# Kernel tuning notes

Hardware: AMD Instinct MI355X
Metric: run time of the kernel (lower is better)

The kernel has to match this reference:

```python
import jax, jax.numpy as jnp
import numpy as np

N_NODE = 100000
HIDDEN = 128
BATCH = 4096
SESS_LEN = 50


def setup_inputs() -> dict:
    key = jax.random.key(0)
    k1, k2, k3, k4, k5 = jax.random.split(key, 5)
    return {
        "item_embedding": jax.random.normal(k1, (N_NODE, HIDDEN), dtype=jnp.float32),
        "items": jax.random.randint(k2, (BATCH, SESS_LEN), 0, N_NODE, dtype=jnp.int64),
        "A": jax.random.uniform(k3, (BATCH, BATCH), dtype=jnp.float32),
        "D": jax.random.uniform(k4, (BATCH, BATCH), dtype=jnp.float32),
        "target_embedding": jax.random.normal(k5, (BATCH, 1, 2 * HIDDEN), dtype=jnp.float32),
    }


def reference(item_embedding, items, A, D, target_embedding):
    # Gather per-session item embeddings: (batch, sess_len, hidden)
    seq_h = item_embedding[items]
    # Sum over session positions -> (batch, hidden)
    relation_emb = jnp.sum(seq_h, axis=1)
    # DA = D @ A, then propagate: (batch, batch) @ (batch, hidden)
    DA = jnp.matmul(D, A)
    relation_emb = jnp.matmul(DA, relation_emb)
    # Row-wise L2 normalization (torch.norm(dim=-1))
    norm = jnp.linalg.norm(relation_emb, axis=-1, keepdims=True)
    return relation_emb / norm
```

## Files before the change

### kernel.cpp

```cpp
#include <hip/hip_runtime.h>
#include <hip/hip_bf16.h>

#define BATCH   4096
#define HIDDEN  128
#define SESS    50
#define KTOT    4096
#define NB      ((size_t)BATCH * HIDDEN)

#define BK      128
#define NT      16
#define ABYTES  16384
#define BBYTES  32768
#define BUF     (ABYTES + BBYTES)

typedef __bf16 bf16x8 __attribute__((ext_vector_type(8)));
typedef __bf16 bf16x4 __attribute__((ext_vector_type(4)));
typedef float  f32x4  __attribute__((ext_vector_type(4)));
typedef float  f32x2  __attribute__((ext_vector_type(2)));

__device__ __forceinline__ f32x4 mfma_bf16(bf16x8 a, bf16x8 b, f32x4 c) {
    return __builtin_amdgcn_mfma_f32_16x16x32_bf16(a, b, c, 0, 0, 0);
}

__device__ __forceinline__ void gload16(const void* g, void* l) {
    __builtin_amdgcn_global_load_lds(
        (const __attribute__((address_space(1))) void*)g,
        (__attribute__((address_space(3))) void*)l, 16, 0, 0);
}


__global__ __launch_bounds__(256)
void gather_sum_kernel(const float* __restrict__ emb,
                       const int* __restrict__ items32,
                       __bf16* __restrict__ ETp) {
    __shared__ int sidx[4][SESS];
    const int t  = threadIdx.x;
    const int b0 = blockIdx.x * 4;
    const bool is64 = (items32[1] | items32[3] | items32[5] | items32[7] |
                       items32[9] | items32[11] | items32[13] | items32[15]) == 0;
    if (t < 4 * SESS) {
        const int w_ = t / SESS, s_ = t % SESS;
        sidx[w_][s_] = is64
            ? (int)((const long long*)items32)[(long)(b0 + w_) * SESS + s_]
            : items32[(b0 + w_) * SESS + s_];
    }
    __syncthreads();
    const int w    = t >> 6;
    const int lane = t & 63;
    const int c    = lane & 31;
    const int h    = lane >> 5;
    f32x4 acc = {0.f, 0.f, 0.f, 0.f};
#pragma unroll
    for (int i = 0; i < 25; ++i) {
        acc += *(const f32x4*)(emb + (long)sidx[w][h + 2 * i] * HIDDEN + c * 4);
    }
#pragma unroll
    for (int j = 0; j < 4; ++j) acc[j] += __shfl_xor(acc[j], 32, 64);
    if (h == 0) {
        const int  b     = b0 + w;
        const long chunk = b >> 3;
        const int  swz   = (int)((chunk & 3) << 4);
        char* basep = (char*)ETp + chunk * 2048 + (b & 7) * 2;
        const int hi4 = (c >> 2) * 256;
#pragma unroll
        for (int j = 0; j < 4; ++j) {
            const int hl = 4 * (c & 3) + j;
            *(__bf16*)(basep + ((hi4 + hl * 16) ^ swz)) = (__bf16)acc[j];
        }
    }
}

__global__ __launch_bounds__(256, 1)
void gemm_mfma_kernel(const float* __restrict__ X,
                      const __bf16* __restrict__ Bpk,
                      float* __restrict__ Tpart) {
    __shared__ __align__(16) char lds[3 * BUF];
    const int tid  = threadIdx.x;
    const int w    = tid >> 6;
    const int lane = tid & 63;
    const int lo   = lane & 15;
    const int quad = lane >> 4;
    const int rowBase = blockIdx.x * 32;
    const int kh      = blockIdx.y;

#define STAGE(t_, dst_) do {                                                 \
    _Pragma("unroll")                                                        \
    for (int ai_ = 0; ai_ < 4; ++ai_) {                                      \
        const int i_    = 4 * w + ai_;                                       \
        const int rloc_ = 2 * i_ + (lane >> 5);                              \
        gload16((const char*)X +                                             \
                    ((size_t)(rowBase + rloc_) * KTOT + kh * 2048 +          \
                     (size_t)(t_) * BK) * 4 +                                \
                    (((lane & 31) * 16) ^ ((rloc_ & 7) << 4)),               \
                (dst_) + i_ * 1024);                                         \
    }                                                                        \
    _Pragma("unroll")                                                        \
    for (int bi_ = 0; bi_ < 8; ++bi_) {                                      \
        const int j_ = 8 * w + bi_;                                          \
        gload16((const char*)Bpk + (size_t)kh * 524288 +                     \
                    (size_t)(t_) * BBYTES + j_ * 1024 + lane * 16,           \
                (dst_) + ABYTES + j_ * 1024);                                \
    }                                                                        \
} while (0)

    f32x4 acc[4];
#pragma unroll
    for (int i = 0; i < 4; ++i) acc[i] = (f32x4){0.f, 0.f, 0.f, 0.f};

    const int rbase = (w & 1) * 16;
    const int ntb   = (w >> 1) * 4;
    const int akey  = (lo & 7) << 4;
    const int bkey  = quad << 4;

#define KTILE(cb_) do {                                                      \
    const char* Ar_ = (cb_) + (rbase + lo) * 512;                            \
    const char* Bb_ = (cb_) + ABYTES + quad * 2048;                          \
    _Pragma("unroll")                                                        \
    for (int ks_ = 0; ks_ < 4; ++ks_) {                                      \
        const f32x4 a0_ =                                                    \
            *(const f32x4*)(Ar_ + ((ks_ * 128 + quad * 32) ^ akey));         \
        const f32x4 a1_ =                                                    \
            *(const f32x4*)(Ar_ + ((ks_ * 128 + quad * 32 + 16) ^ akey));    \
        bf16x8 af_;                                                          \
        af_[0] = (__bf16)a0_[0]; af_[1] = (__bf16)a0_[1];                    \
        af_[2] = (__bf16)a0_[2]; af_[3] = (__bf16)a0_[3];                    \
        af_[4] = (__bf16)a1_[0]; af_[5] = (__bf16)a1_[1];                    \
        af_[6] = (__bf16)a1_[2]; af_[7] = (__bf16)a1_[3];                    \
        _Pragma("unroll")                                                    \
        for (int j_ = 0; j_ < 4; ++j_) {                                     \
            const bf16x8 b_ = *(const bf16x8*)(Bb_ + ks_ * 8192 +            \
                (((ntb + j_) * 256 + lo * 16) ^ bkey));                      \
            acc[j_] = mfma_bf16(af_, b_, acc[j_]);                           \
        }                                                                    \
    }                                                                        \
} while (0)

    STAGE(0, lds);
    STAGE(1, lds + BUF);

    char* cb = lds;
    char* sb = lds + 2 * BUF;
    for (int t = 0; t < NT; ++t) {
        if (t + 2 < NT) STAGE(t + 2, sb);
        if (t < NT - 2)
            asm volatile("s_waitcnt vmcnt(24)" ::: "memory");
        else if (t == NT - 2)
            asm volatile("s_waitcnt vmcnt(12)" ::: "memory");
        else
            asm volatile("s_waitcnt vmcnt(0)" ::: "memory");
        __builtin_amdgcn_s_barrier();
        __builtin_amdgcn_sched_barrier(0);
        KTILE(cb);
        __builtin_amdgcn_s_barrier();
        __builtin_amdgcn_sched_barrier(0);
        cb += BUF; if (cb == lds + 3 * BUF) cb = lds;
        sb += BUF; if (sb == lds + 3 * BUF) sb = lds;
    }
#undef KTILE
#undef STAGE

    float* op = Tpart + (size_t)kh * NB +
                (size_t)(rowBase + rbase) * HIDDEN;
#pragma unroll
    for (int r = 0; r < 4; ++r) {
#pragma unroll
        for (int j = 0; j < 4; ++j)
            op[(quad * 4 + r) * HIDDEN + (ntb + j) * 16 + lo] = acc[j][r];
    }
}

__global__ __launch_bounds__(256)
void reduce2_kernel(const float* __restrict__ Tp, __bf16* __restrict__ TTp) {
    const size_t i = ((size_t)blockIdx.x * 256 + threadIdx.x) * 4;
    f32x4 a = *(const f32x4*)(Tp + i);
    a += *(const f32x4*)(Tp + NB + i);
    const int  b     = (int)(i >> 7);
    const int  h0    = (int)(i & 127);
    const long chunk = b >> 3;
    const int  swz   = (int)((chunk & 3) << 4);
    char* basep = (char*)TTp + chunk * 2048 + (b & 7) * 2;
#pragma unroll
    for (int j = 0; j < 4; ++j) {
        const int h = h0 + j;
        *(__bf16*)(basep + (((h >> 4) * 256 + (h & 15) * 16) ^ swz)) =
            (__bf16)a[j];
    }
}

__global__ __launch_bounds__(256)
void reduce_norm_kernel(const float* __restrict__ Tp, float* __restrict__ out) {
    const int t    = threadIdx.x;
    const int w    = t >> 6;
    const int lane = t & 63;
    const int row  = blockIdx.x * 4 + w;
    const size_t base = (size_t)row * HIDDEN + lane * 2;
    f32x2 v = *(const f32x2*)(Tp + base);
    v += *(const f32x2*)(Tp + NB + base);
    float sq = v[0] * v[0] + v[1] * v[1];
#pragma unroll
    for (int m = 1; m < 64; m <<= 1) sq += __shfl_xor(sq, m, 64);
    const float s = rsqrtf(sq);
    f32x2 o = {v[0] * s, v[1] * s};
    *(f32x2*)(out + base) = o;
}

extern "C" void kernel_launch(void* const* d_in, const int* in_sizes, int n_in,
                              void* d_out, int out_size, void* d_ws, size_t ws_size,
                              hipStream_t stream) {
    const float* emb   = (const float*)d_in[0];
    const int*   items = (const int*)d_in[1];
    const float* A     = (const float*)d_in[2];
    const float* D     = (const float*)d_in[3];
    float* out = (float*)d_out;

    __bf16* ETp = (__bf16*)d_ws;
    __bf16* TTp = ETp + NB;
    float*  Tp  = (float*)(TTp + NB);

    gather_sum_kernel<<<BATCH / 4, 256, 0, stream>>>(emb, items, ETp);
    gemm_mfma_kernel<<<dim3(BATCH / 32, 2), 256, 0, stream>>>(A, ETp, Tp);
    reduce2_kernel<<<512, 256, 0, stream>>>(Tp, TTp);
    gemm_mfma_kernel<<<dim3(BATCH / 32, 2), 256, 0, stream>>>(D, TTp, Tp);
    reduce_norm_kernel<<<BATCH / 4, 256, 0, stream>>>(Tp, out);
}
```

Before: 209.8 us.

## Retile GEMM to 64-row blocks with four-way split-K and 64-wide K tiles

Each GEMM workgroup now covers 64 rows instead of 32, and every wave computes a full 16x128 output strip. K is split four ways instead of two, and the K tile shrinks to 64, so each staged buffer holds less data. Each B tile loaded into LDS is now reused by twice as many rows, while the grid stays at 256 workgroups. In exchange the split-K partials double, so the reduce and normalize kernels read four partial buffers, which adds global memory traffic and workspace.

```diff
diff --git a/kernel.cpp b/kernel.cpp
--- a/kernel.cpp
+++ b/kernel.cpp
@@ -7,14 +7,15 @@
 #define KTOT    4096
 #define NB      ((size_t)BATCH * HIDDEN)
 
-#define BK      128
-#define NT      16
+#define MB      64
+#define KQ      1024
+#define BK      64
+#define NT      (KQ / BK)
 #define ABYTES  16384
-#define BBYTES  32768
+#define BBYTES  16384
 #define BUF     (ABYTES + BBYTES)
 
 typedef __bf16 bf16x8 __attribute__((ext_vector_type(8)));
-typedef __bf16 bf16x4 __attribute__((ext_vector_type(4)));
 typedef float  f32x4  __attribute__((ext_vector_type(4)));
 typedef float  f32x2  __attribute__((ext_vector_type(2)));
 
@@ -80,43 +81,41 @@
     const int lane = tid & 63;
     const int lo   = lane & 15;
     const int quad = lane >> 4;
-    const int rowBase = blockIdx.x * 32;
-    const int kh      = blockIdx.y;
+    const int rowBase = blockIdx.x * MB;
+    const int kq      = blockIdx.y;
 
 #define STAGE(t_, dst_) do {                                                 \
     _Pragma("unroll")                                                        \
     for (int ai_ = 0; ai_ < 4; ++ai_) {                                      \
-        const int i_    = 4 * w + ai_;                                       \
-        const int rloc_ = 2 * i_ + (lane >> 5);                              \
+        const int i_  = 4 * w + ai_;                                         \
+        const int rl_ = 4 * i_ + (lane >> 4);           \
         gload16((const char*)X +                                             \
-                    ((size_t)(rowBase + rloc_) * KTOT + kh * 2048 +          \
+                    ((size_t)(rowBase + rl_) * KTOT + kq * KQ +              \
                      (size_t)(t_) * BK) * 4 +                                \
-                    (((lane & 31) * 16) ^ ((rloc_ & 7) << 4)),               \
+                    (((lane & 15) * 16) ^ ((rl_ & 7) << 4)),                 \
                 (dst_) + i_ * 1024);                                         \
     }                                                                        \
     _Pragma("unroll")                                                        \
-    for (int bi_ = 0; bi_ < 8; ++bi_) {                                      \
-        const int j_ = 8 * w + bi_;                                          \
-        gload16((const char*)Bpk + (size_t)kh * 524288 +                     \
+    for (int bi_ = 0; bi_ < 4; ++bi_) {                                      \
+        const int j_ = 4 * w + bi_;                                          \
+        gload16((const char*)Bpk + (size_t)kq * (KQ * 256) +                 \
                     (size_t)(t_) * BBYTES + j_ * 1024 + lane * 16,           \
                 (dst_) + ABYTES + j_ * 1024);                                \
     }                                                                        \
 } while (0)
 
-    f32x4 acc[4];
-#pragma unroll
-    for (int i = 0; i < 4; ++i) acc[i] = (f32x4){0.f, 0.f, 0.f, 0.f};
-
-    const int rbase = (w & 1) * 16;
-    const int ntb   = (w >> 1) * 4;
-    const int akey  = (lo & 7) << 4;
-    const int bkey  = quad << 4;
+    f32x4 acc[8];
+#pragma unroll
+    for (int i = 0; i < 8; ++i) acc[i] = (f32x4){0.f, 0.f, 0.f, 0.f};
+
+    const int akey = (lo & 7) << 4;
+    const int bkey = quad << 4;
 
 #define KTILE(cb_) do {                                                      \
-    const char* Ar_ = (cb_) + (rbase + lo) * 512;                            \
+    const char* Ar_ = (cb_) + (16 * w + lo) * 256;                           \
     const char* Bb_ = (cb_) + ABYTES + quad * 2048;                          \
     _Pragma("unroll")                                                        \
-    for (int ks_ = 0; ks_ < 4; ++ks_) {                                      \
+    for (int ks_ = 0; ks_ < 2; ++ks_) {                                      \
         const f32x4 a0_ =                                                    \
             *(const f32x4*)(Ar_ + ((ks_ * 128 + quad * 32) ^ akey));         \
         const f32x4 a1_ =                                                    \
@@ -127,9 +126,9 @@
         af_[4] = (__bf16)a1_[0]; af_[5] = (__bf16)a1_[1];                    \
         af_[6] = (__bf16)a1_[2]; af_[7] = (__bf16)a1_[3];                    \
         _Pragma("unroll")                                                    \
-        for (int j_ = 0; j_ < 4; ++j_) {                                     \
+        for (int j_ = 0; j_ < 8; ++j_) {                                     \
             const bf16x8 b_ = *(const bf16x8*)(Bb_ + ks_ * 8192 +            \
-                (((ntb + j_) * 256 + lo * 16) ^ bkey));                      \
+                ((j_ * 256 + lo * 16) ^ bkey));                              \
             acc[j_] = mfma_bf16(af_, b_, acc[j_]);                           \
         }                                                                    \
     }                                                                        \
@@ -143,9 +142,9 @@
     for (int t = 0; t < NT; ++t) {
         if (t + 2 < NT) STAGE(t + 2, sb);
         if (t < NT - 2)
-            asm volatile("s_waitcnt vmcnt(24)" ::: "memory");
+            asm volatile("s_waitcnt vmcnt(16)" ::: "memory");
         else if (t == NT - 2)
-            asm volatile("s_waitcnt vmcnt(12)" ::: "memory");
+            asm volatile("s_waitcnt vmcnt(8)" ::: "memory");
         else
             asm volatile("s_waitcnt vmcnt(0)" ::: "memory");
         __builtin_amdgcn_s_barrier();
@@ -159,21 +158,23 @@
 #undef KTILE
 #undef STAGE
 
-    float* op = Tpart + (size_t)kh * NB +
-                (size_t)(rowBase + rbase) * HIDDEN;
+    float* op = Tpart + (size_t)kq * NB +
+                (size_t)(rowBase + 16 * w) * HIDDEN;
 #pragma unroll
     for (int r = 0; r < 4; ++r) {
 #pragma unroll
-        for (int j = 0; j < 4; ++j)
-            op[(quad * 4 + r) * HIDDEN + (ntb + j) * 16 + lo] = acc[j][r];
+        for (int j = 0; j < 8; ++j)
+            op[(quad * 4 + r) * HIDDEN + j * 16 + lo] = acc[j][r];
     }
 }
 
 __global__ __launch_bounds__(256)
-void reduce2_kernel(const float* __restrict__ Tp, __bf16* __restrict__ TTp) {
+void reduce4_kernel(const float* __restrict__ Tp, __bf16* __restrict__ TTp) {
     const size_t i = ((size_t)blockIdx.x * 256 + threadIdx.x) * 4;
     f32x4 a = *(const f32x4*)(Tp + i);
     a += *(const f32x4*)(Tp + NB + i);
+    a += *(const f32x4*)(Tp + 2 * NB + i);
+    a += *(const f32x4*)(Tp + 3 * NB + i);
     const int  b     = (int)(i >> 7);
     const int  h0    = (int)(i & 127);
     const long chunk = b >> 3;
@@ -196,6 +197,8 @@
     const size_t base = (size_t)row * HIDDEN + lane * 2;
     f32x2 v = *(const f32x2*)(Tp + base);
     v += *(const f32x2*)(Tp + NB + base);
+    v += *(const f32x2*)(Tp + 2 * NB + base);
+    v += *(const f32x2*)(Tp + 3 * NB + base);
     float sq = v[0] * v[0] + v[1] * v[1];
 #pragma unroll
     for (int m = 1; m < 64; m <<= 1) sq += __shfl_xor(sq, m, 64);
@@ -218,8 +221,8 @@
     float*  Tp  = (float*)(TTp + NB);
 
     gather_sum_kernel<<<BATCH / 4, 256, 0, stream>>>(emb, items, ETp);
-    gemm_mfma_kernel<<<dim3(BATCH / 32, 2), 256, 0, stream>>>(A, ETp, Tp);
-    reduce2_kernel<<<512, 256, 0, stream>>>(Tp, TTp);
-    gemm_mfma_kernel<<<dim3(BATCH / 32, 2), 256, 0, stream>>>(D, TTp, Tp);
+    gemm_mfma_kernel<<<dim3(BATCH / MB, 4), 256, 0, stream>>>(A, ETp, Tp);
+    reduce4_kernel<<<512, 256, 0, stream>>>(Tp, TTp);
+    gemm_mfma_kernel<<<dim3(BATCH / MB, 4), 256, 0, stream>>>(D, TTp, Tp);
     reduce_norm_kernel<<<BATCH / 4, 256, 0, stream>>>(Tp, out);
 }
```

Measured after the change: 217.6 us. 3.7% more time.
